# Kernel optimization log

Hardware: AMD Instinct MI355X
Metric: run time of the kernel (lower is better)

Reference implementation:

```python
import jax, jax.numpy as jnp
import numpy as np

B, H, W, C = 64, 56, 56, 192
NH, WS, SS = 6, 7, 3          # heads, window size, shift size
N = WS * WS                   # tokens per window = 49
NW = (H // WS) * (W // WS)    # windows per image = 64
HD = C // NH                  # head dim = 32
SCALE = HD ** -0.5
EPS = 1e-5


def _rel_pos_index():
    coords = np.stack(np.meshgrid(np.arange(WS), np.arange(WS), indexing='ij'))  # [2,WS,WS]
    flat = coords.reshape(2, -1)                                                  # [2,N]
    rel = (flat[:, :, None] - flat[:, None, :]).transpose(1, 2, 0)                # [N,N,2]
    rel[..., 0] += WS - 1
    rel[..., 1] += WS - 1
    rel[..., 0] *= 2 * WS - 1
    return jnp.asarray(rel.sum(-1))  # [N,N] int

REL_IDX = _rel_pos_index()


def _shift_mask():
    # standard Swin shifted-window attention mask: 0 within region, -100 across
    img = np.zeros((H, W), dtype=np.float32)
    cnt = 0
    for hs in (slice(0, -WS), slice(-WS, -SS), slice(-SS, None)):
        for ws in (slice(0, -WS), slice(-WS, -SS), slice(-SS, None)):
            img[hs, ws] = cnt
            cnt += 1
    win = img.reshape(H // WS, WS, W // WS, WS).transpose(0, 2, 1, 3).reshape(NW, N)
    diff = win[:, None, :] - win[:, :, None]
    return jnp.asarray(np.where(diff != 0, -100.0, 0.0).astype(np.float32))  # [NW,N,N]


def setup_inputs() -> dict:
    key = jax.random.key(0)
    ks = jax.random.split(key, 8)
    s = 0.02
    return {
        'x': jax.random.normal(ks[0], (B, H, W, C), jnp.float32),
        'mask_matrix': _shift_mask(),
        'norm1_g': jnp.ones((C,), jnp.float32),
        'norm1_b': jnp.zeros((C,), jnp.float32),
        'qkv_w': jax.random.normal(ks[1], (3 * C, C), jnp.float32) * s,
        'qkv_b': jnp.zeros((3 * C,), jnp.float32),
        'rpb_table': jax.random.normal(ks[2], ((2 * WS - 1) ** 2, NH), jnp.float32) * s,
        'proj_w': jax.random.normal(ks[3], (C, C), jnp.float32) * s,
        'proj_b': jnp.zeros((C,), jnp.float32),
        'norm2_g': jnp.ones((C,), jnp.float32),
        'norm2_b': jnp.zeros((C,), jnp.float32),
        'fc1_w': jax.random.normal(ks[4], (4 * C, C), jnp.float32) * s,
        'fc1_b': jnp.zeros((4 * C,), jnp.float32),
        'fc2_w': jax.random.normal(ks[5], (C, 4 * C), jnp.float32) * s,
        'fc2_b': jnp.zeros((C,), jnp.float32),
    }


def _ln(x, g, b):
    m = jnp.mean(x, axis=-1, keepdims=True)
    v = jnp.mean(jnp.square(x - m), axis=-1, keepdims=True)
    return (x - m) * jax.lax.rsqrt(v + EPS) * g + b


def _block(x, mask_matrix, norm1_g, norm1_b, qkv_w, qkv_b, rpb_table,
           proj_w, proj_b, norm2_g, norm2_b, fc1_w, fc1_b, fc2_w, fc2_b):
    shortcut = x
    xn = _ln(x, norm1_g, norm1_b)
    # cyclic shift
    xs = jnp.roll(xn, (-SS, -SS), axis=(1, 2))
    # window partition -> [B*NW, N, C]
    win = xs.reshape(B, H // WS, WS, W // WS, WS, C).transpose(0, 1, 3, 2, 4, 5).reshape(B * NW, N, C)
    # qkv projection
    qkv = jnp.einsum('wnc,dc->wnd', win, qkv_w) + qkv_b           # [B*NW, N, 3C]
    qkv = qkv.reshape(B * NW, N, 3, NH, HD).transpose(2, 0, 3, 1, 4)
    q, k, v = qkv[0], qkv[1], qkv[2]                               # [B*NW, NH, N, HD]
    attn = jnp.einsum('whqd,whkd->whqk', q * SCALE, k)             # [B*NW, NH, N, N]
    # relative position bias gather
    bias = rpb_table[REL_IDX.reshape(-1)].reshape(N, N, NH).transpose(2, 0, 1)  # [NH,N,N]
    attn = attn + bias[None]
    # shifted-window mask
    attn = attn.reshape(B, NW, NH, N, N) + mask_matrix[None, :, None]
    attn = jax.nn.softmax(attn.reshape(B * NW, NH, N, N), axis=-1)
    out = jnp.einsum('whqk,whkd->whqd', attn, v)                   # [B*NW, NH, N, HD]
    out = out.transpose(0, 2, 1, 3).reshape(B * NW, N, C)
    out = jnp.einsum('wnc,dc->wnd', out, proj_w) + proj_b
    # window reverse + reverse shift
    xr = out.reshape(B, H // WS, W // WS, WS, WS, C).transpose(0, 1, 3, 2, 4, 5).reshape(B, H, W, C)
    xr = jnp.roll(xr, (SS, SS), axis=(1, 2))
    x = shortcut + xr
    # MLP
    xn2 = _ln(x, norm2_g, norm2_b)
    h = jax.nn.gelu(jnp.einsum('bhwc,dc->bhwd', xn2, fc1_w) + fc1_b, approximate=False)
    x = x + jnp.einsum('bhwd,cd->bhwc', h, fc2_w) + fc2_b
    return x


def reference(x, mask_matrix, norm1_g, norm1_b, qkv_w, qkv_b, rpb_table,
              proj_w, proj_b, norm2_g, norm2_b, fc1_w, fc1_b, fc2_w, fc2_b):
    return _block(x, mask_matrix, norm1_g, norm1_b, qkv_w, qkv_b, rpb_table,
                  proj_w, proj_b, norm2_g, norm2_b, fc1_w, fc1_b, fc2_w, fc2_b)
```

## Files before the change

kernel.cpp:

```cpp
#include <hip/hip_runtime.h>
#include <hip/hip_bf16.h>
#include <math.h>

typedef __attribute__((ext_vector_type(8))) short s16x8;
typedef __attribute__((ext_vector_type(4))) float f32x4;

static constexpr float cSCALE = 0.17677669529663687f;

__device__ __forceinline__ float bf2f(unsigned short u) {
    union { unsigned int i; float f; } c; c.i = ((unsigned int)u) << 16; return c.f;
}
__device__ __forceinline__ unsigned short f2bf(float f) {
    union { float f; unsigned int i; } c; c.f = f;
    unsigned int r = c.i + (0x7fffu + ((c.i >> 16) & 1u));
    return (unsigned short)(r >> 16);
}
__device__ __forceinline__ unsigned pk2(float a, float b) {
    unsigned r;
    asm("v_cvt_pk_bf16_f32 %0, %1, %2" : "=v"(r) : "v"(a), "v"(b));
    return r;
}
__device__ __forceinline__ s16x8 cvt8(const float4 a, const float4 b) {
    s16x8 r;
    r[0]=(short)f2bf(a.x); r[1]=(short)f2bf(a.y); r[2]=(short)f2bf(a.z); r[3]=(short)f2bf(a.w);
    r[4]=(short)f2bf(b.x); r[5]=(short)f2bf(b.y); r[6]=(short)f2bf(b.z); r[7]=(short)f2bf(b.w);
    return r;
}
__device__ __forceinline__ float gelu_f(float t) {
    const float u = 1.5957691216057308f * t * (1.0f + 0.044715f * t * t);
    return t / (1.0f + __expf(-u));
}

#define GLDS16(gp, lp) __builtin_amdgcn_global_load_lds( \
    (const __attribute__((address_space(1))) void*)(gp), \
    (__attribute__((address_space(3))) void*)(lp), 16, 0, 0)

__device__ __forceinline__ void ln_frag(const float* __restrict__ rowp,
                                        const float* __restrict__ g,
                                        const float* __restrict__ b,
                                        int hi, s16x8* xa)
{
    float4 v[12];
    #pragma unroll
    for (int k = 0; k < 6; ++k) {
        v[2*k]   = *(const float4*)(rowp + k*32 + hi*8);
        v[2*k+1] = *(const float4*)(rowp + k*32 + hi*8 + 4);
    }
    float sm = 0.f, sq = 0.f;
    #pragma unroll
    for (int i = 0; i < 12; ++i) {
        sm += (v[i].x + v[i].y) + (v[i].z + v[i].w);
        sq += (v[i].x*v[i].x + v[i].y*v[i].y) + (v[i].z*v[i].z + v[i].w*v[i].w);
    }
    sm += __shfl_xor(sm, 16); sq += __shfl_xor(sq, 16);
    sm += __shfl_xor(sm, 32); sq += __shfl_xor(sq, 32);
    const float mean = sm * (1.0f/192.0f);
    const float rstd = rsqrtf(sq * (1.0f/192.0f) - mean*mean + 1e-5f);
    #pragma unroll
    for (int k = 0; k < 6; ++k) {
        const float4 ga = *(const float4*)(g + k*32 + hi*8);
        const float4 gb = *(const float4*)(g + k*32 + hi*8 + 4);
        const float4 ba = *(const float4*)(b + k*32 + hi*8);
        const float4 bb = *(const float4*)(b + k*32 + hi*8 + 4);
        union { s16x8 s; unsigned u[4]; } r;
        r.u[0] = pk2((v[2*k].x  -mean)*rstd*ga.x + ba.x, (v[2*k].y  -mean)*rstd*ga.y + ba.y);
        r.u[1] = pk2((v[2*k].z  -mean)*rstd*ga.z + ba.z, (v[2*k].w  -mean)*rstd*ga.w + ba.w);
        r.u[2] = pk2((v[2*k+1].x-mean)*rstd*gb.x + bb.x, (v[2*k+1].y-mean)*rstd*gb.y + bb.y);
        r.u[3] = pk2((v[2*k+1].z-mean)*rstd*gb.z + bb.z, (v[2*k+1].w-mean)*rstd*gb.w + bb.w);
        xa[k] = r.s;
    }
}

__global__ __launch_bounds__(256)
void pack_all(const float* __restrict__ qkvw, const float* __restrict__ pw,
              const float* __restrict__ f1w, const float* __restrict__ f2w,
              const float* __restrict__ mask, const float* __restrict__ rpb,
              unsigned short* __restrict__ o, unsigned short* __restrict__ ob)
{
    if (blockIdx.x < 216) {
        const int t = blockIdx.x * 256 + threadIdx.x;
        const int lane = t & 63, f = t >> 6;
        const int ln = lane & 15, ko = (lane >> 4) * 8;
        const float* src;
        if (f < 216) {
            const int h = f / 36, r = f - h * 36, nf = r / 6, kf = r - nf * 6;
            src = qkvw + (size_t)((nf >> 1) * 192 + h * 32 + (nf & 1) * 16 + ln) * 192 + kf * 32 + ko;
        } else if (f < 288) {
            const int g = f - 216, h = g / 12, nf = g - h * 12;
            src = pw + (size_t)(nf * 16 + ln) * 192 + h * 32 + ko;
        } else {
            const int g = f - 288;
            const int c = g / 24, r24 = g - c * 24;
            if (r24 < 12) {
                const int nf = r24 / 6, kf = r24 - nf * 6;
                src = f1w + (size_t)(c * 32 + nf * 16 + ln) * 192 + kf * 32 + ko;
            } else {
                const int nf = r24 - 12;
                src = f2w + (size_t)(nf * 16 + ln) * 768 + c * 32 + ko;
            }
        }
        *(s16x8*)(o + (size_t)t * 8) = cvt8(*(const float4*)src, *(const float4*)(src + 4));
    } else {
        const int bid = blockIdx.x - 216;
        const int wi = bid / 6, h = bid - wi * 6;
        for (int t = threadIdx.x; t < 49 * 64; t += 256) {
            const int n = t >> 6, mm = t & 63;
            const int ln = mm >> 2, nf = mm & 3;
            const int m = nf * 16 + ln;
            float v = -100.0f;
            if (m < 49) {
                const int p1 = n / 7, q1 = n - p1 * 7, p2 = m / 7, q2 = m - p2 * 7;
                const int ridx = (p1 - p2 + 6) * 13 + (q1 - q2 + 6);
                v = rpb[ridx * 6 + h] + mask[(size_t)wi * 2401 + n * 49 + m];
            }
            ob[(size_t)(wi * 6 + h) * 3136 + t] = f2bf(v);
        }
    }
}

__global__ __launch_bounds__(256, 4)
void swin_attn(const float* __restrict__ x, const float* __restrict__ g1,
               const float* __restrict__ b1, const unsigned short* __restrict__ wp,
               const unsigned short* __restrict__ bias_g,
               const float* __restrict__ qkvb, const float* __restrict__ pb,
               float* __restrict__ y)
{
    __shared__ __align__(16) unsigned short q_[64][40];
    __shared__ __align__(16) unsigned short o_[64][40];
    __shared__ __align__(16) unsigned short k2_[2][64][40];
    __shared__ __align__(16) unsigned short vt2_[2][32][72];
    __shared__ __align__(16) unsigned short p_[64][72];

    const s16x8* wv = (const s16x8*)wp;
    const int w  = blockIdx.x;
    const int bb = w >> 6, wi = w & 63;
    const int wh = wi >> 3, ww = wi & 7;
    const int tid = threadIdx.x, lane = tid & 63, wave = tid >> 6;
    const int ln = lane & 15, hi = lane >> 4, ko = hi * 8, ro = hi * 4;
    const int m0 = wave * 16;

    s16x8 xa[6];
    {
        const int t = m0 + ln;
        const int p = t / 7, q7 = t - p * 7;
        int i2 = wh * 7 + p + 3;  if (i2 >= 56) i2 -= 56;
        int j2 = ww * 7 + q7 + 3; if (j2 >= 56) j2 -= 56;
        const float* xr = x + ((size_t)(bb * 56 + i2) * 56 + j2) * 192;
        ln_frag(xr, g1, b1, hi, xa);
        if (t >= 49) {
            #pragma unroll
            for (int k = 0; k < 6; ++k) xa[k] = s16x8{0,0,0,0,0,0,0,0};
        }
    }

    auto qkv_head = [&](int hh) {
        const s16x8* wq = wv + ((size_t)(hh * 36) << 6);
        #pragma unroll
        for (int nf = 0; nf < 6; ++nf) {
            s16x8 bf6[6];
            #pragma unroll
            for (int kf = 0; kf < 6; ++kf) bf6[kf] = wq[(nf * 6 + kf) * 64 + lane];
            f32x4 a = f32x4{0.f,0.f,0.f,0.f};
            #pragma unroll
            for (int kf = 0; kf < 6; ++kf)
                a = __builtin_amdgcn_mfma_f32_16x16x32_bf16(xa[kf], bf6[kf], a, 0, 0, 0);
            const int col = nf * 16 + ln;
            if (nf < 2) {
                const float bq = qkvb[hh*32 + col];
                const unsigned lo = pk2((a[0]+bq)*cSCALE, (a[1]+bq)*cSCALE);
                const unsigned hh2 = pk2((a[2]+bq)*cSCALE, (a[3]+bq)*cSCALE);
                q_[m0+ro+0][col] = (unsigned short)lo;  q_[m0+ro+1][col] = (unsigned short)(lo >> 16);
                q_[m0+ro+2][col] = (unsigned short)hh2; q_[m0+ro+3][col] = (unsigned short)(hh2 >> 16);
            } else if (nf < 4) {
                const float bk = qkvb[192 + hh*32 + col - 32];
                const unsigned lo = pk2(a[0]+bk, a[1]+bk), hh2 = pk2(a[2]+bk, a[3]+bk);
                k2_[hh&1][m0+ro+0][col-32] = (unsigned short)lo;  k2_[hh&1][m0+ro+1][col-32] = (unsigned short)(lo >> 16);
                k2_[hh&1][m0+ro+2][col-32] = (unsigned short)hh2; k2_[hh&1][m0+ro+3][col-32] = (unsigned short)(hh2 >> 16);
            } else {
                const float bv = qkvb[384 + hh*32 + col - 64];
                const unsigned lo = pk2(a[0]+bv, a[1]+bv), hh2 = pk2(a[2]+bv, a[3]+bv);
                vt2_[hh&1][col-64][m0+ro+0] = (unsigned short)lo;  vt2_[hh&1][col-64][m0+ro+1] = (unsigned short)(lo >> 16);
                vt2_[hh&1][col-64][m0+ro+2] = (unsigned short)hh2; vt2_[hh&1][col-64][m0+ro+3] = (unsigned short)(hh2 >> 16);
            }
        }
    };

    qkv_head(0);

    f32x4 accp[12];
    #pragma unroll
    for (int i = 0; i < 12; ++i) accp[i] = f32x4{0.f,0.f,0.f,0.f};

    uint2 bb4[4];
    {
        const unsigned short* bg = bias_g + (size_t)(wi * 6) * 3136;
        #pragma unroll
        for (int i = 0; i < 4; ++i) {
            const int nc = min(m0 + ro + i, 48);
            bb4[i] = *(const uint2*)(bg + nc * 64 + ln * 4);
        }
    }

    for (int h = 0; h < 6; ++h) {
        __syncthreads();

        f32x4 s4[4];
        {
            const s16x8 aq = *(const s16x8*)&q_[m0 + ln][ko];
            #pragma unroll
            for (int nf = 0; nf < 4; ++nf) {
                const s16x8 bk = *(const s16x8*)&k2_[h & 1][nf * 16 + ln][ko];
                s4[nf] = __builtin_amdgcn_mfma_f32_16x16x32_bf16(aq, bk, f32x4{0.f,0.f,0.f,0.f}, 0, 0, 0);
            }
        }
        float inv4[4];
        #pragma unroll
        for (int i = 0; i < 4; ++i) {
            const int n = m0 + ro + i;
            const uint2 u = bb4[i];
            const float e0 = __expf(s4[0][i] + bf2f((unsigned short)(u.x)));
            const float e1 = __expf(s4[1][i] + bf2f((unsigned short)(u.x >> 16)));
            const float e2 = __expf(s4[2][i] + bf2f((unsigned short)(u.y)));
            const float e3 = __expf(s4[3][i] + bf2f((unsigned short)(u.y >> 16)));
            float ssum = (e0 + e1) + (e2 + e3);
            #pragma unroll
            for (int o = 1; o < 16; o <<= 1) ssum += __shfl_xor(ssum, o);
            inv4[i] = 1.0f / ssum;
            const unsigned plo = pk2(e0, e1), phi = pk2(e2, e3);
            p_[n][     ln] = (unsigned short)plo;
            p_[n][16 + ln] = (unsigned short)(plo >> 16);
            p_[n][32 + ln] = (unsigned short)phi;
            p_[n][48 + ln] = (unsigned short)(phi >> 16);
        }

        {
            const int hn = (h < 5) ? h + 1 : 5;
            const unsigned short* bg = bias_g + (size_t)(wi * 6 + hn) * 3136;
            #pragma unroll
            for (int i = 0; i < 4; ++i) {
                const int nc = min(m0 + ro + i, 48);
                bb4[i] = *(const uint2*)(bg + nc * 64 + ln * 4);
            }
        }

        f32x4 o2[2];
        o2[0] = f32x4{0.f,0.f,0.f,0.f}; o2[1] = f32x4{0.f,0.f,0.f,0.f};
        #pragma unroll
        for (int kf = 0; kf < 2; ++kf) {
            const s16x8 ap = *(const s16x8*)&p_[m0 + ln][kf * 32 + ko];
            #pragma unroll
            for (int nf = 0; nf < 2; ++nf) {
                const s16x8 bv = *(const s16x8*)&vt2_[h & 1][nf * 16 + ln][kf * 32 + ko];
                o2[nf] = __builtin_amdgcn_mfma_f32_16x16x32_bf16(ap, bv, o2[nf], 0, 0, 0);
            }
        }
        #pragma unroll
        for (int nf = 0; nf < 2; ++nf) {
            const int col = nf * 16 + ln;
            const unsigned lo = pk2(o2[nf][0] * inv4[0], o2[nf][1] * inv4[1]);
            const unsigned hh2 = pk2(o2[nf][2] * inv4[2], o2[nf][3] * inv4[3]);
            o_[m0+ro+0][col] = (unsigned short)lo;  o_[m0+ro+1][col] = (unsigned short)(lo >> 16);
            o_[m0+ro+2][col] = (unsigned short)hh2; o_[m0+ro+3][col] = (unsigned short)(hh2 >> 16);
        }

        if (h < 5) qkv_head(h + 1);

        {
            const s16x8 ao = *(const s16x8*)&o_[m0 + ln][ko];
            const s16x8* wpj = wv + ((size_t)(216 + h * 12) << 6);
            #pragma unroll
            for (int half = 0; half < 2; ++half) {
                s16x8 bf6[6];
                #pragma unroll
                for (int nf = 0; nf < 6; ++nf) bf6[nf] = wpj[(half * 6 + nf) * 64 + lane];
                #pragma unroll
                for (int nf = 0; nf < 6; ++nf)
                    accp[half * 6 + nf] = __builtin_amdgcn_mfma_f32_16x16x32_bf16(
                        ao, bf6[nf], accp[half * 6 + nf], 0, 0, 0);
            }
        }
    }

    #pragma unroll
    for (int i = 0; i < 4; ++i) {
        const int n = m0 + ro + i;
        if (n < 49) {
            const int p = n / 7, q7 = n - p * 7;
            int i2 = wh * 7 + p + 3;  if (i2 >= 56) i2 -= 56;
            int j2 = ww * 7 + q7 + 3; if (j2 >= 56) j2 -= 56;
            const size_t base = ((size_t)(bb * 56 + i2) * 56 + j2) * 192;
            #pragma unroll
            for (int nf = 0; nf < 12; ++nf) {
                const int col = nf * 16 + ln;
                y[base + col] = x[base + col] + pb[col] + accp[nf][i];
            }
        }
    }
}

__device__ __forceinline__ void stage24k(const unsigned short* __restrict__ wp, int c,
                                         unsigned short* dst, int tid) {
    const unsigned short* g = wp + (((size_t)(288 + c * 24)) << 9) + tid * 8;
    unsigned short* l = dst + tid * 8;
    #pragma unroll
    for (int i = 0; i < 6; ++i)
        GLDS16(g + i * 2048, l + i * 2048);
}

__global__ __launch_bounds__(256, 2)
void swin_mlp(const float* __restrict__ g2, const float* __restrict__ b2,
              const unsigned short* __restrict__ wp,
              const float* __restrict__ f1b, const float* __restrict__ f2b,
              float* __restrict__ y)
{
    __shared__ __align__(16) unsigned short wbuf[2][12288];
    __shared__ __align__(16) unsigned short hb[128][40];
    __shared__ float f1b_l[768];
    __shared__ float f2b_l[192];

    const int tid = threadIdx.x, lane = tid & 63, wave = tid >> 6;
    const int ln = lane & 15, hi = lane >> 4, ko = hi * 8, ro = hi * 4;
    const int m0 = wave * 32;
    const size_t r0 = (size_t)blockIdx.x * 128;

    for (int t = tid; t < 768; t += 256) f1b_l[t] = f1b[t];
    for (int t = tid; t < 192; t += 256) f2b_l[t] = f2b[t];

    s16x8 xa[12];
    ln_frag(y + (r0 + m0 +      ln) * 192, g2, b2, hi, xa);
    ln_frag(y + (r0 + m0 + 16 + ln) * 192, g2, b2, hi, xa + 6);

    stage24k(wp, 0, wbuf[0], tid);
    stage24k(wp, 1, wbuf[1], tid);
    asm volatile("s_waitcnt lgkmcnt(0)" ::: "memory");

    f32x4 acc2[24];
    #pragma unroll
    for (int i = 0; i < 24; ++i) acc2[i] = f32x4{0.f,0.f,0.f,0.f};

    for (int c = 0; c < 24; ++c) {
        if (c == 23) asm volatile("s_waitcnt vmcnt(0)" ::: "memory");
        else         asm volatile("s_waitcnt vmcnt(6)" ::: "memory");
        __builtin_amdgcn_s_barrier();

        const s16x8* wb = (const s16x8*)wbuf[c & 1];
        f32x4 acc1[4];
        #pragma unroll
        for (int i = 0; i < 4; ++i) acc1[i] = f32x4{0.f,0.f,0.f,0.f};
        #pragma unroll
        for (int kf = 0; kf < 6; ++kf) {
            #pragma unroll
            for (int nf = 0; nf < 2; ++nf) {
                const s16x8 b = wb[(nf * 6 + kf) * 64 + lane];
                acc1[nf*2+0] = __builtin_amdgcn_mfma_f32_16x16x32_bf16(xa[kf],     b, acc1[nf*2+0], 0, 0, 0);
                acc1[nf*2+1] = __builtin_amdgcn_mfma_f32_16x16x32_bf16(xa[6 + kf], b, acc1[nf*2+1], 0, 0, 0);
            }
        }
        #pragma unroll
        for (int nf = 0; nf < 2; ++nf) {
            const int col = nf * 16 + ln;
            const float bias = f1b_l[c * 32 + col];
            #pragma unroll
            for (int rs = 0; rs < 2; ++rs) {
                const f32x4 a = acc1[nf*2+rs];
                const int rb = m0 + rs * 16 + ro;
                const unsigned lo = pk2(gelu_f(a[0] + bias), gelu_f(a[1] + bias));
                const unsigned hh2 = pk2(gelu_f(a[2] + bias), gelu_f(a[3] + bias));
                hb[rb+0][col] = (unsigned short)lo;  hb[rb+1][col] = (unsigned short)(lo >> 16);
                hb[rb+2][col] = (unsigned short)hh2; hb[rb+3][col] = (unsigned short)(hh2 >> 16);
            }
        }
        const s16x8 ah0 = *(const s16x8*)&hb[m0 +      ln][ko];
        const s16x8 ah1 = *(const s16x8*)&hb[m0 + 16 + ln][ko];
        #pragma unroll
        for (int nf = 0; nf < 12; ++nf) {
            const s16x8 b = wb[(12 + nf) * 64 + lane];
            acc2[nf*2+0] = __builtin_amdgcn_mfma_f32_16x16x32_bf16(ah0, b, acc2[nf*2+0], 0, 0, 0);
            acc2[nf*2+1] = __builtin_amdgcn_mfma_f32_16x16x32_bf16(ah1, b, acc2[nf*2+1], 0, 0, 0);
        }

        if (c < 23) {
            __builtin_amdgcn_s_barrier();
            if (c < 22) stage24k(wp, c + 2, wbuf[c & 1], tid);
        }
    }

    #pragma unroll
    for (int rs = 0; rs < 2; ++rs) {
        #pragma unroll
        for (int i = 0; i < 4; ++i) {
            const int row = m0 + rs * 16 + ro + i;
            float* yp = y + (r0 + row) * 192;
            #pragma unroll
            for (int nf = 0; nf < 12; ++nf) {
                const int col = nf * 16 + ln;
                yp[col] = yp[col] + f2b_l[col] + acc2[nf*2+rs][i];
            }
        }
    }
}

extern "C" void kernel_launch(void* const* d_in, const int* in_sizes, int n_in,
                              void* d_out, int out_size, void* d_ws, size_t ws_size,
                              hipStream_t stream) {
    (void)in_sizes; (void)n_in; (void)ws_size; (void)out_size;
    const float* x    = (const float*)d_in[0];
    const float* mask = (const float*)d_in[1];
    const float* g1   = (const float*)d_in[2];
    const float* b1   = (const float*)d_in[3];
    const float* qkvw = (const float*)d_in[4];
    const float* qkvb = (const float*)d_in[5];
    const float* rpb  = (const float*)d_in[6];
    const float* pw   = (const float*)d_in[7];
    const float* pb   = (const float*)d_in[8];
    const float* g2   = (const float*)d_in[9];
    const float* b2   = (const float*)d_in[10];
    const float* f1w  = (const float*)d_in[11];
    const float* f1b  = (const float*)d_in[12];
    const float* f2w  = (const float*)d_in[13];
    const float* f2b  = (const float*)d_in[14];
    float* y = (float*)d_out;
    unsigned short* wpk  = (unsigned short*)d_ws;
    unsigned short* bias = wpk + 442368;

    pack_all<<<dim3(600), dim3(256), 0, stream>>>(qkvw, pw, f1w, f2w, mask, rpb, wpk, bias);
    swin_attn<<<dim3(64 * 64), dim3(256), 0, stream>>>(
        x, g1, b1, wpk, bias, qkvb, pb, y);
    swin_mlp<<<dim3(1568), dim3(256), 0, stream>>>(
        g2, b2, wpk, f1b, f2b, y);
}
```

Measured before the change: 525.7 us.

## Stage QKV and projection weights into LDS with a double-buffered async pipeline

Each head's work is split into four stages: three QKV column-group stages and one attention-plus-projection stage. The weight slice for each stage is copied into a double-buffered LDS buffer with global-to-LDS loads, issued two stages ahead. This replaces per-wave register loads of weights from global memory, which each of the four waves repeated. It drops the double-buffered K/V storage and the min-occupancy launch bound. In exchange it adds about 24 KB of LDS and two barriers per stage, and it removes the earlier overlap of the next head's QKV with the current head's attention.

```diff
diff --git a/kernel.cpp b/kernel.cpp
--- a/kernel.cpp
+++ b/kernel.cpp
@@ -118,7 +118,7 @@
     }
 }
 
-__global__ __launch_bounds__(256, 4)
+__global__ __launch_bounds__(256)
 void swin_attn(const float* __restrict__ x, const float* __restrict__ g1,
                const float* __restrict__ b1, const unsigned short* __restrict__ wp,
                const unsigned short* __restrict__ bias_g,
@@ -127,11 +127,11 @@
 {
     __shared__ __align__(16) unsigned short q_[64][40];
     __shared__ __align__(16) unsigned short o_[64][40];
-    __shared__ __align__(16) unsigned short k2_[2][64][40];
-    __shared__ __align__(16) unsigned short vt2_[2][32][72];
+    __shared__ __align__(16) unsigned short k_[64][40];
+    __shared__ __align__(16) unsigned short vt_[32][72];
     __shared__ __align__(16) unsigned short p_[64][72];
-
-    const s16x8* wv = (const s16x8*)wp;
+    __shared__ __align__(16) unsigned short wbuf[2][6144];
+
     const int w  = blockIdx.x;
     const int bb = w >> 6, wi = w & 63;
     const int wh = wi >> 3, ww = wi & 7;
@@ -153,89 +153,36 @@
         }
     }
 
-    auto qkv_head = [&](int hh) {
-        const s16x8* wq = wv + ((size_t)(hh * 36) << 6);
-        #pragma unroll
-        for (int nf = 0; nf < 6; ++nf) {
-            s16x8 bf6[6];
-            #pragma unroll
-            for (int kf = 0; kf < 6; ++kf) bf6[kf] = wq[(nf * 6 + kf) * 64 + lane];
-            f32x4 a = f32x4{0.f,0.f,0.f,0.f};
-            #pragma unroll
-            for (int kf = 0; kf < 6; ++kf)
-                a = __builtin_amdgcn_mfma_f32_16x16x32_bf16(xa[kf], bf6[kf], a, 0, 0, 0);
-            const int col = nf * 16 + ln;
-            if (nf < 2) {
-                const float bq = qkvb[hh*32 + col];
-                const unsigned lo = pk2((a[0]+bq)*cSCALE, (a[1]+bq)*cSCALE);
-                const unsigned hh2 = pk2((a[2]+bq)*cSCALE, (a[3]+bq)*cSCALE);
-                q_[m0+ro+0][col] = (unsigned short)lo;  q_[m0+ro+1][col] = (unsigned short)(lo >> 16);
-                q_[m0+ro+2][col] = (unsigned short)hh2; q_[m0+ro+3][col] = (unsigned short)(hh2 >> 16);
-            } else if (nf < 4) {
-                const float bk = qkvb[192 + hh*32 + col - 32];
-                const unsigned lo = pk2(a[0]+bk, a[1]+bk), hh2 = pk2(a[2]+bk, a[3]+bk);
-                k2_[hh&1][m0+ro+0][col-32] = (unsigned short)lo;  k2_[hh&1][m0+ro+1][col-32] = (unsigned short)(lo >> 16);
-                k2_[hh&1][m0+ro+2][col-32] = (unsigned short)hh2; k2_[hh&1][m0+ro+3][col-32] = (unsigned short)(hh2 >> 16);
-            } else {
-                const float bv = qkvb[384 + hh*32 + col - 64];
-                const unsigned lo = pk2(a[0]+bv, a[1]+bv), hh2 = pk2(a[2]+bv, a[3]+bv);
-                vt2_[hh&1][col-64][m0+ro+0] = (unsigned short)lo;  vt2_[hh&1][col-64][m0+ro+1] = (unsigned short)(lo >> 16);
-                vt2_[hh&1][col-64][m0+ro+2] = (unsigned short)hh2; vt2_[hh&1][col-64][m0+ro+3] = (unsigned short)(hh2 >> 16);
-            }
-        }
+    auto stageS = [&](int s) {
+        const int h = s >> 2, g = s & 3;
+        const int fid = (g < 3) ? (h * 36 + g * 12) : (216 + h * 12);
+        const unsigned short* gp = wp + ((size_t)fid << 9) + tid * 8;
+        unsigned short* lp = wbuf[s & 1] + tid * 8;
+        GLDS16(gp, lp);
+        GLDS16(gp + 2048, lp + 2048);
+        GLDS16(gp + 4096, lp + 4096);
     };
 
-    qkv_head(0);
+    stageS(0);
+    stageS(1);
 
     f32x4 accp[12];
     #pragma unroll
     for (int i = 0; i < 12; ++i) accp[i] = f32x4{0.f,0.f,0.f,0.f};
 
+    const int nclamp = min(m0 + ro, 48);
+    (void)nclamp;
     uint2 bb4[4];
-    {
-        const unsigned short* bg = bias_g + (size_t)(wi * 6) * 3136;
-        #pragma unroll
-        for (int i = 0; i < 4; ++i) {
-            const int nc = min(m0 + ro + i, 48);
-            bb4[i] = *(const uint2*)(bg + nc * 64 + ln * 4);
-        }
-    }
-
-    for (int h = 0; h < 6; ++h) {
-        __syncthreads();
-
-        f32x4 s4[4];
-        {
-            const s16x8 aq = *(const s16x8*)&q_[m0 + ln][ko];
-            #pragma unroll
-            for (int nf = 0; nf < 4; ++nf) {
-                const s16x8 bk = *(const s16x8*)&k2_[h & 1][nf * 16 + ln][ko];
-                s4[nf] = __builtin_amdgcn_mfma_f32_16x16x32_bf16(aq, bk, f32x4{0.f,0.f,0.f,0.f}, 0, 0, 0);
-            }
-        }
-        float inv4[4];
-        #pragma unroll
-        for (int i = 0; i < 4; ++i) {
-            const int n = m0 + ro + i;
-            const uint2 u = bb4[i];
-            const float e0 = __expf(s4[0][i] + bf2f((unsigned short)(u.x)));
-            const float e1 = __expf(s4[1][i] + bf2f((unsigned short)(u.x >> 16)));
-            const float e2 = __expf(s4[2][i] + bf2f((unsigned short)(u.y)));
-            const float e3 = __expf(s4[3][i] + bf2f((unsigned short)(u.y >> 16)));
-            float ssum = (e0 + e1) + (e2 + e3);
-            #pragma unroll
-            for (int o = 1; o < 16; o <<= 1) ssum += __shfl_xor(ssum, o);
-            inv4[i] = 1.0f / ssum;
-            const unsigned plo = pk2(e0, e1), phi = pk2(e2, e3);
-            p_[n][     ln] = (unsigned short)plo;
-            p_[n][16 + ln] = (unsigned short)(plo >> 16);
-            p_[n][32 + ln] = (unsigned short)phi;
-            p_[n][48 + ln] = (unsigned short)(phi >> 16);
-        }
-
-        {
-            const int hn = (h < 5) ? h + 1 : 5;
-            const unsigned short* bg = bias_g + (size_t)(wi * 6 + hn) * 3136;
+
+    for (int s = 0; s < 24; ++s) {
+        const int h = s >> 2, g = s & 3;
+        if (s >= 22) asm volatile("s_waitcnt vmcnt(0)" ::: "memory");
+        else         asm volatile("s_waitcnt vmcnt(3)" ::: "memory");
+        __builtin_amdgcn_s_barrier();
+        const s16x8* wb = (const s16x8*)wbuf[s & 1];
+
+        if (g == 0) {
+            const unsigned short* bg = bias_g + (size_t)(wi * 6 + h) * 3136;
             #pragma unroll
             for (int i = 0; i < 4; ++i) {
                 const int nc = min(m0 + ro + i, 48);
@@ -243,42 +190,95 @@
             }
         }
 
-        f32x4 o2[2];
-        o2[0] = f32x4{0.f,0.f,0.f,0.f}; o2[1] = f32x4{0.f,0.f,0.f,0.f};
-        #pragma unroll
-        for (int kf = 0; kf < 2; ++kf) {
-            const s16x8 ap = *(const s16x8*)&p_[m0 + ln][kf * 32 + ko];
+        if (g < 3) {
+            #pragma unroll
+            for (int j = 0; j < 2; ++j) {
+                f32x4 a = f32x4{0.f,0.f,0.f,0.f};
+                #pragma unroll
+                for (int kf = 0; kf < 6; ++kf)
+                    a = __builtin_amdgcn_mfma_f32_16x16x32_bf16(
+                        xa[kf], wb[(j * 6 + kf) * 64 + lane], a, 0, 0, 0);
+                const int nf = 2 * g + j;
+                const int col = nf * 16 + ln;
+                if (nf < 2) {
+                    const float bq = qkvb[h*32 + col];
+                    const unsigned lo = pk2((a[0]+bq)*cSCALE, (a[1]+bq)*cSCALE);
+                    const unsigned hh2 = pk2((a[2]+bq)*cSCALE, (a[3]+bq)*cSCALE);
+                    q_[m0+ro+0][col] = (unsigned short)lo;  q_[m0+ro+1][col] = (unsigned short)(lo >> 16);
+                    q_[m0+ro+2][col] = (unsigned short)hh2; q_[m0+ro+3][col] = (unsigned short)(hh2 >> 16);
+                } else if (nf < 4) {
+                    const float bk = qkvb[192 + h*32 + col - 32];
+                    const unsigned lo = pk2(a[0]+bk, a[1]+bk), hh2 = pk2(a[2]+bk, a[3]+bk);
+                    k_[m0+ro+0][col-32] = (unsigned short)lo;  k_[m0+ro+1][col-32] = (unsigned short)(lo >> 16);
+                    k_[m0+ro+2][col-32] = (unsigned short)hh2; k_[m0+ro+3][col-32] = (unsigned short)(hh2 >> 16);
+                } else {
+                    const float bv = qkvb[384 + h*32 + col - 64];
+                    const unsigned lo = pk2(a[0]+bv, a[1]+bv), hh2 = pk2(a[2]+bv, a[3]+bv);
+                    vt_[col-64][m0+ro+0] = (unsigned short)lo;  vt_[col-64][m0+ro+1] = (unsigned short)(lo >> 16);
+                    vt_[col-64][m0+ro+2] = (unsigned short)hh2; vt_[col-64][m0+ro+3] = (unsigned short)(hh2 >> 16);
+                }
+            }
+        } else {
+            f32x4 s4[4];
+            {
+                const s16x8 aq = *(const s16x8*)&q_[m0 + ln][ko];
+                #pragma unroll
+                for (int nf = 0; nf < 4; ++nf) {
+                    const s16x8 bk = *(const s16x8*)&k_[nf * 16 + ln][ko];
+                    s4[nf] = __builtin_amdgcn_mfma_f32_16x16x32_bf16(aq, bk, f32x4{0.f,0.f,0.f,0.f}, 0, 0, 0);
+                }
+            }
+            float inv4[4];
+            #pragma unroll
+            for (int i = 0; i < 4; ++i) {
+                const int n = m0 + ro + i;
+                const uint2 u = bb4[i];
+                const float e0 = __expf(s4[0][i] + bf2f((unsigned short)(u.x)));
+                const float e1 = __expf(s4[1][i] + bf2f((unsigned short)(u.x >> 16)));
+                const float e2 = __expf(s4[2][i] + bf2f((unsigned short)(u.y)));
+                const float e3 = __expf(s4[3][i] + bf2f((unsigned short)(u.y >> 16)));
+                float ssum = (e0 + e1) + (e2 + e3);
+                #pragma unroll
+                for (int o = 1; o < 16; o <<= 1) ssum += __shfl_xor(ssum, o);
+                inv4[i] = 1.0f / ssum;
+                const unsigned plo = pk2(e0, e1), phi = pk2(e2, e3);
+                p_[n][     ln] = (unsigned short)plo;
+                p_[n][16 + ln] = (unsigned short)(plo >> 16);
+                p_[n][32 + ln] = (unsigned short)phi;
+                p_[n][48 + ln] = (unsigned short)(phi >> 16);
+            }
+
+            f32x4 o2[2];
+            o2[0] = f32x4{0.f,0.f,0.f,0.f}; o2[1] = f32x4{0.f,0.f,0.f,0.f};
+            #pragma unroll
+            for (int kf = 0; kf < 2; ++kf) {
+                const s16x8 ap = *(const s16x8*)&p_[m0 + ln][kf * 32 + ko];
+                #pragma unroll
+                for (int nf = 0; nf < 2; ++nf) {
+                    const s16x8 bv = *(const s16x8*)&vt_[nf * 16 + ln][kf * 32 + ko];
+                    o2[nf] = __builtin_amdgcn_mfma_f32_16x16x32_bf16(ap, bv, o2[nf], 0, 0, 0);
+                }
+            }
             #pragma unroll
             for (int nf = 0; nf < 2; ++nf) {
-                const s16x8 bv = *(const s16x8*)&vt2_[h & 1][nf * 16 + ln][kf * 32 + ko];
-                o2[nf] = __builtin_amdgcn_mfma_f32_16x16x32_bf16(ap, bv, o2[nf], 0, 0, 0);
-            }
-        }
-        #pragma unroll
-        for (int nf = 0; nf < 2; ++nf) {
-            const int col = nf * 16 + ln;
-            const unsigned lo = pk2(o2[nf][0] * inv4[0], o2[nf][1] * inv4[1]);
-            const unsigned hh2 = pk2(o2[nf][2] * inv4[2], o2[nf][3] * inv4[3]);
-            o_[m0+ro+0][col] = (unsigned short)lo;  o_[m0+ro+1][col] = (unsigned short)(lo >> 16);
-            o_[m0+ro+2][col] = (unsigned short)hh2; o_[m0+ro+3][col] = (unsigned short)(hh2 >> 16);
-        }
-
-        if (h < 5) qkv_head(h + 1);
-
-        {
-            const s16x8 ao = *(const s16x8*)&o_[m0 + ln][ko];
-            const s16x8* wpj = wv + ((size_t)(216 + h * 12) << 6);
-            #pragma unroll
-            for (int half = 0; half < 2; ++half) {
-                s16x8 bf6[6];
+                const int col = nf * 16 + ln;
+                const unsigned lo = pk2(o2[nf][0] * inv4[0], o2[nf][1] * inv4[1]);
+                const unsigned hh2 = pk2(o2[nf][2] * inv4[2], o2[nf][3] * inv4[3]);
+                o_[m0+ro+0][col] = (unsigned short)lo;  o_[m0+ro+1][col] = (unsigned short)(lo >> 16);
+                o_[m0+ro+2][col] = (unsigned short)hh2; o_[m0+ro+3][col] = (unsigned short)(hh2 >> 16);
+            }
+
+            {
+                const s16x8 ao = *(const s16x8*)&o_[m0 + ln][ko];
                 #pragma unroll
-                for (int nf = 0; nf < 6; ++nf) bf6[nf] = wpj[(half * 6 + nf) * 64 + lane];
-                #pragma unroll
-                for (int nf = 0; nf < 6; ++nf)
-                    accp[half * 6 + nf] = __builtin_amdgcn_mfma_f32_16x16x32_bf16(
-                        ao, bf6[nf], accp[half * 6 + nf], 0, 0, 0);
-            }
-        }
+                for (int nf = 0; nf < 12; ++nf)
+                    accp[nf] = __builtin_amdgcn_mfma_f32_16x16x32_bf16(
+                        ao, wb[nf * 64 + lane], accp[nf], 0, 0, 0);
+            }
+        }
+
+        __builtin_amdgcn_s_barrier();
+        if (s < 22) stageS(s + 2);
     }
 
     #pragma unroll
```

Measured after the change: 557.2 us. +6.0%, slower.
